# Kernel optimization log

Hardware: AMD Instinct MI355X
Metric: run time of the kernel (lower is better)

The kernel has to match this reference:

```python
import jax, jax.numpy as jnp
import numpy as np

N_HEADS = 16
D_MODEL = 1024
TOTAL = 8192
N_SEQ = 8
SEQ_LEN = TOTAL // N_SEQ


def setup_inputs() -> dict:
    key = jax.random.key(0)
    ks = jax.random.split(key, 12)
    f = jnp.float32
    d = D_MODEL
    inp = {
        "query": jax.random.normal(ks[0], (TOTAL, d), f),
        "key": jax.random.normal(ks[1], (TOTAL, d), f),
        "value": jax.random.normal(ks[2], (TOTAL, d), f),
        "seq_lengths_q": jnp.full((N_SEQ,), SEQ_LEN, jnp.int64 if jax.config.jax_enable_x64 else jnp.int32),
        "seq_lengths_kv": jnp.full((N_SEQ,), SEQ_LEN, jnp.int64 if jax.config.jax_enable_x64 else jnp.int32),
        "Wq": jax.random.normal(ks[3], (d, d), f) * 0.02,
        "bq": jnp.zeros((d,), f),
        "Wk": jax.random.normal(ks[4], (d, d), f) * 0.02,
        "bk": jnp.zeros((d,), f),
        "Wv": jax.random.normal(ks[5], (d, d), f) * 0.02,
        "bv": jnp.zeros((d,), f),
        "Wo": jax.random.normal(ks[6], (d, d), f) * 0.02,
        "bo": jnpp if False else jnp.zeros((d,), f),
    }
    return inp


def reference(query, key, value, seq_lengths_q, seq_lengths_kv, Wq, bq, Wk, bk, Wv, bv, Wo, bo):
    Tq, d = query.shape
    Tkv = key.shape[0]
    H = N_HEADS
    Dh = d // H
    B = seq_lengths_q.shape[0]
    Lq = Tq // B  # equal-length packed sequences
    Lkv = Tkv // B
    scale = 1.0 / jnp.sqrt(jnp.asarray(Dh, query.dtype))

    # torch Linear: x @ W.T + b
    Q = (query @ Wq.T + bq).reshape(H, Tq, Dh)   # NOTE: raw view, no transpose
    K = (key @ Wk.T + bk).reshape(H, Tkv, Dh)    # (replicates original's view semantics)
    V = (value @ Wv.T + bv).reshape(H, Tkv, Dh)

    # Block-diagonal mask over equal-length sequences == per-block attention.
    Qb = Q.reshape(H, B, Lq, Dh)
    Kb = K.reshape(H, B, Lkv, Dh)
    Vb = V.reshape(H, B, Lkv, Dh)

    scores = jnp.einsum("hbqd,hbkd->hbqk", Qb, Kb) * scale  # [H,B,Lq,Lkv]
    probs = jax.nn.softmax(scores, axis=-1)
    attn = jnp.einsum("hbqk,hbkd->hbqd", probs, Vb)          # [H,B,Lq,Dh]

    attn = attn.reshape(H, Tq, Dh).reshape(Tq, d)  # matches .view(total_q, d_model)
    out = attn @ Wo.T + bo
    return out
```

## Files before the change

kernel.cpp:

```cpp
#include <hip/hip_runtime.h>
#include <hip/hip_bf16.h>

#define TOTAL   8192
#define DMODEL  1024
#define NHEADS  16
#define NSEQ    8
#define DH      64

typedef float  f32x4 __attribute__((ext_vector_type(4)));
typedef short  s16x8 __attribute__((ext_vector_type(8)));
typedef unsigned short u16;
typedef u16    u16x8 __attribute__((ext_vector_type(8)));
typedef unsigned u32x2 __attribute__((ext_vector_type(2)));

__device__ __forceinline__ u16 f2bf_rne(float x) {
  union { float f; unsigned u; } v; v.f = x;
  unsigned r = v.u + 0x7FFFu + ((v.u >> 16) & 1u);
  return (u16)(r >> 16);
}

__device__ __forceinline__ void async_cp16(const u16* g, u16* l) {
  __builtin_amdgcn_global_load_lds(
      (const __attribute__((address_space(1))) unsigned int*)g,
      (__attribute__((address_space(3))) unsigned int*)l, 16, 0, 0);
}

__device__ __forceinline__ void cvt8_one(const float* __restrict__ src,
                                         u16* __restrict__ dst, long i) {
  float4 a = *reinterpret_cast<const float4*>(src + i);
  float4 b = *reinterpret_cast<const float4*>(src + i + 4);
  u16x8 o;
  o[0] = f2bf_rne(a.x); o[1] = f2bf_rne(a.y); o[2] = f2bf_rne(a.z); o[3] = f2bf_rne(a.w);
  o[4] = f2bf_rne(b.x); o[5] = f2bf_rne(b.y); o[6] = f2bf_rne(b.z); o[7] = f2bf_rne(b.w);
  *reinterpret_cast<u16x8*>(dst + i) = o;
}

__global__ __launch_bounds__(256) void cvt8(const float* __restrict__ src,
                                            u16* __restrict__ dst) {
  cvt8_one(src, dst, ((long)blockIdx.x * 256 + threadIdx.x) * 8);
}

__global__ __launch_bounds__(256) void cvt8_w4(const float* __restrict__ w0,
                                               const float* __restrict__ w1,
                                               const float* __restrict__ w2,
                                               const float* __restrict__ w3,
                                               u16* __restrict__ dst) {
  const float* srcs[4] = {w0, w1, w2, w3};
  cvt8_one(srcs[blockIdx.y], dst + (long)blockIdx.y * (DMODEL * (long)DMODEL),
           ((long)blockIdx.x * 256 + threadIdx.x) * 8);
}

__global__ __launch_bounds__(256) void cvt8_x3(const float* __restrict__ x0,
                                               const float* __restrict__ x1,
                                               const float* __restrict__ x2,
                                               u16* __restrict__ dst) {
  const float* srcs[3] = {x0, x1, x2};
  cvt8_one(srcs[blockIdx.y], dst + (long)blockIdx.y * (TOTAL * (long)DMODEL),
           ((long)blockIdx.x * 256 + threadIdx.x) * 8);
}

template<bool OUT_BF16>
__device__ __forceinline__ void gemm256_core(const u16* __restrict__ A,
                                             const u16* __restrict__ B,
                                             const float* __restrict__ bias,
                                             void* __restrict__ Cp,
                                             long bm0, long bn0, u16* lds) {
  const int tid  = threadIdx.x;
  const int lane = tid & 63;
  const int wv   = tid >> 6;
  const int quad = lane >> 4;
  const int m16  = lane & 15;
  const int wm   = (wv >> 1) * 64;
  const int wn   = (wv & 1) * 64;

  const int l8   = lane >> 3;
  const int slot = (lane & 7) ^ l8;
  const long g_lane = (long)l8 * DMODEL + slot * 8;
  const u16* Ap = A + (bm0 + wv * 32) * (long)DMODEL + g_lane;
  const u16* Bp = B + (bn0 + wv * 16) * (long)DMODEL + g_lane;
  u16* ldsA = lds + wv * (4 * 512);
  u16* ldsB = lds + 16384 + wv * (2 * 512);

  const int swz0 = ((quad * 16)      ^ ((m16 & 7) << 4)) >> 1;
  const int swz1 = ((64 + quad * 16) ^ ((m16 & 7) << 4)) >> 1;
  const int aro = (wm + m16) * 64;
  const int bro = 16384 + (wn + m16) * 64;

  f32x4 acc[4][4] = {};

#define STAGE_A(buf, kt) do {                                       \
    _Pragma("unroll")                                               \
    for (int al = 0; al < 4; al++)                                  \
      async_cp16(Ap + (long)(kt) * 64 + al * (8 * DMODEL),          \
                 ldsA + (buf) * 24576 + al * 512);                  \
  } while (0)
#define STAGE_B(buf, kt) do {                                       \
    _Pragma("unroll")                                               \
    for (int bl = 0; bl < 2; bl++)                                  \
      async_cp16(Bp + (long)(kt) * 64 + bl * (8 * DMODEL),          \
                 ldsB + (buf) * 24576 + bl * 512);                  \
  } while (0)

  STAGE_A(0, 0); STAGE_B(0, 0);
  STAGE_A(1, 1); STAGE_B(1, 1);

  #pragma unroll
  for (int t = 0; t < 16; t++) {
    const int cur = t % 3;
    const int stg = (t + 2) % 3;
    if (t < 15) asm volatile("s_waitcnt vmcnt(6)" ::: "memory");
    else        asm volatile("s_waitcnt vmcnt(0)" ::: "memory");
    __builtin_amdgcn_s_barrier();
    asm volatile("" ::: "memory");

    const u16* lb = lds + cur * 24576;

    if (t < 14) STAGE_A(stg, t + 2);
    s16x8 bf[4][2], af[2][2];
    #pragma unroll
    for (int n = 0; n < 4; n++) {
      bf[n][0] = *(const s16x8*)&lb[bro + n * 1024 + swz0];
      bf[n][1] = *(const s16x8*)&lb[bro + n * 1024 + swz1];
    }
    #pragma unroll
    for (int i = 0; i < 2; i++) {
      af[i][0] = *(const s16x8*)&lb[aro + i * 1024 + swz0];
      af[i][1] = *(const s16x8*)&lb[aro + i * 1024 + swz1];
    }
    asm volatile("s_waitcnt lgkmcnt(0)" ::: "memory");
    __builtin_amdgcn_sched_barrier(0);
    __builtin_amdgcn_s_setprio(1);
    #pragma unroll
    for (int i = 0; i < 2; i++)
      #pragma unroll
      for (int n = 0; n < 4; n++) {
        acc[i][n] = __builtin_amdgcn_mfma_f32_16x16x32_bf16(af[i][0], bf[n][0], acc[i][n], 0, 0, 0);
        acc[i][n] = __builtin_amdgcn_mfma_f32_16x16x32_bf16(af[i][1], bf[n][1], acc[i][n], 0, 0, 0);
      }
    __builtin_amdgcn_s_setprio(0);
    __builtin_amdgcn_s_barrier();

    if (t < 14) STAGE_B(stg, t + 2);
    s16x8 ag[2][2];
    #pragma unroll
    for (int i = 0; i < 2; i++) {
      ag[i][0] = *(const s16x8*)&lb[aro + (i + 2) * 1024 + swz0];
      ag[i][1] = *(const s16x8*)&lb[aro + (i + 2) * 1024 + swz1];
    }
    asm volatile("s_waitcnt lgkmcnt(0)" ::: "memory");
    __builtin_amdgcn_sched_barrier(0);
    __builtin_amdgcn_s_setprio(1);
    #pragma unroll
    for (int i = 0; i < 2; i++)
      #pragma unroll
      for (int n = 0; n < 4; n++) {
        acc[i + 2][n] = __builtin_amdgcn_mfma_f32_16x16x32_bf16(ag[i][0], bf[n][0], acc[i + 2][n], 0, 0, 0);
        acc[i + 2][n] = __builtin_amdgcn_mfma_f32_16x16x32_bf16(ag[i][1], bf[n][1], acc[i + 2][n], 0, 0, 0);
      }
    __builtin_amdgcn_s_setprio(0);
  }
#undef STAGE_A
#undef STAGE_B

  #pragma unroll
  for (int n = 0; n < 4; n++) {
    const long col = bn0 + wn + n * 16 + m16;
    const float bj = bias[col];
    #pragma unroll
    for (int i = 0; i < 4; i++) {
      const long row0 = bm0 + wm + i * 16 + quad * 4;
      #pragma unroll
      for (int r = 0; r < 4; r++) {
        float v = acc[i][n][r] + bj;
        if constexpr (OUT_BF16)
          ((u16*)Cp)[(row0 + r) * DMODEL + col] = f2bf_rne(v);
        else
          ((float*)Cp)[(row0 + r) * DMODEL + col] = v;
      }
    }
  }
}

__device__ __forceinline__ void decode_wg(int x, long& bm0, long& bn0) {
  const int wg = (x & 7) * 32 + (x >> 3);
  bm0 = (long)(wg >> 3) * 256;
  bn0 = (long)(wg & 7) * 128;
}

template<bool OUT_BF16>
__global__ __launch_bounds__(512, 2) void gemm256_nt(const u16* __restrict__ A,
                                                     const u16* __restrict__ B,
                                                     const float* __restrict__ bias,
                                                     void* __restrict__ Cp) {
  __shared__ __align__(1024) u16 lds[3 * 24576];
  long bm0, bn0;
  decode_wg(blockIdx.x, bm0, bn0);
  gemm256_core<OUT_BF16>(A, B, bias, Cp, bm0, bn0, lds);
}

__global__ __launch_bounds__(512, 2) void gemm256_qkv(const u16* __restrict__ X3,
                                                      const u16* __restrict__ W3,
                                                      const float* __restrict__ bq,
                                                      const float* __restrict__ bk,
                                                      const float* __restrict__ bv,
                                                      u16* __restrict__ QKV) {
  __shared__ __align__(1024) u16 lds[3 * 24576];
  const int z = blockIdx.y;
  const float* bias = (z == 0) ? bq : (z == 1) ? bk : bv;
  long bm0, bn0;
  decode_wg(blockIdx.x, bm0, bn0);
  gemm256_core<true>(X3 + (long)z * (TOTAL * (long)DMODEL),
                     W3 + (long)z * (DMODEL * (long)DMODEL),
                     bias,
                     QKV + (long)z * (TOTAL * (long)DMODEL),
                     bm0, bn0, lds);
}

__global__ __launch_bounds__(256) void transpose_v(const u16* __restrict__ Vbf,
                                                   u16* __restrict__ Vt) {
  constexpr int TP = 72;
  __shared__ u16 tile[64 * TP];
  const int tid = threadIdx.x;
  const long base = (long)blockIdx.y * 65536;
  const int kt = blockIdx.x;
  {
    int k = tid >> 2, dh0 = (tid & 3) * 16;
    const u16* g = Vbf + base + (long)(kt * 64 + k) * 64 + dh0;
    u16x8 a = ((const u16x8*)g)[0];
    u16x8 b = ((const u16x8*)g)[1];
    #pragma unroll
    for (int i = 0; i < 8; i++) tile[(dh0 + i) * TP + k] = a[i];
    #pragma unroll
    for (int i = 0; i < 8; i++) tile[(dh0 + 8 + i) * TP + k] = b[i];
  }
  __syncthreads();
  {
    int dh = tid >> 2, k0 = (tid & 3) * 16;
    u16x8 a = *(const u16x8*)&tile[dh * TP + k0];
    u16x8 b = *(const u16x8*)&tile[dh * TP + k0 + 8];
    u16* g = Vt + base + (long)dh * 1024 + kt * 64 + k0;
    ((u16x8*)g)[0] = a;
    ((u16x8*)g)[1] = b;
  }
}

__global__ __launch_bounds__(256) void attn_kernel(const u16* __restrict__ Qbf,
                                                   const u16* __restrict__ Kbf,
                                                   const u16* __restrict__ Vt,
                                                   u16* __restrict__ Obf) {
  constexpr int KP = 72;
  __shared__ u16 Ks[64 * KP];
  __shared__ u16 Vs[64 * KP];
  __shared__ u16 Es[4 * 32 * KP];
  const int tid  = threadIdx.x;
  const int lane = tid & 63;
  const int wv   = tid >> 6;
  const int quad = lane >> 4;
  const int m16  = lane & 15;
  const int qt   = blockIdx.y;
  const long base = (long)blockIdx.x * 65536;

  const int qrow0 = qt * 128 + wv * 32;
  s16x8 aq[2][2];
  #pragma unroll
  for (int g = 0; g < 2; g++)
    #pragma unroll
    for (int s = 0; s < 2; s++)
      aq[g][s] = *(const s16x8*)(Qbf + base + (long)(qrow0 + g * 16 + m16) * 64 + s * 32 + quad * 8);

  f32x4 acc_o[2][4] = {};
  f32x4 acc_d[2] = {};

  union { u16x8 u; s16x8 s; } onesu;
  u16 ov = (m16 == 0) ? (u16)0x3F80 : (u16)0;
  #pragma unroll
  for (int i = 0; i < 8; i++) onesu.u[i] = ov;
  const s16x8 bones = onesu.s;

  const float SC = 0.125f * 1.44269504088896340736f;
  const int sr = tid >> 2;
  const int sk = (tid & 3) * 16;

  const u16* gK = Kbf + base + (long)sr * 64 + sk;
  const u16* gV = Vt  + base + (long)sr * 1024 + sk;
  u16x8 kra = ((const u16x8*)gK)[0], krb = ((const u16x8*)gK)[1];
  u16x8 vra = ((const u16x8*)gV)[0], vrb = ((const u16x8*)gV)[1];

  for (int nt = 0; nt < 16; nt++) {
    *(u16x8*)&Ks[sr * KP + sk]     = kra;
    *(u16x8*)&Ks[sr * KP + sk + 8] = krb;
    *(u16x8*)&Vs[sr * KP + sk]     = vra;
    *(u16x8*)&Vs[sr * KP + sk + 8] = vrb;
    __syncthreads();
    if (nt < 15) {
      const u16* nK = gK + (nt + 1) * 4096;
      const u16* nV = gV + (nt + 1) * 64;
      kra = ((const u16x8*)nK)[0]; krb = ((const u16x8*)nK)[1];
      vra = ((const u16x8*)nV)[0]; vrb = ((const u16x8*)nV)[1];
    }

    #pragma unroll
    for (int mt = 0; mt < 4; mt++) {
      const int krow = (mt * 16 + m16) * KP;
      s16x8 kf0 = *(const s16x8*)&Ks[krow + quad * 8];
      s16x8 kf1 = *(const s16x8*)&Ks[krow + 32 + quad * 8];
      #pragma unroll
      for (int g = 0; g < 2; g++) {
        f32x4 s = {0.f, 0.f, 0.f, 0.f};
        s = __builtin_amdgcn_mfma_f32_16x16x32_bf16(kf0, aq[g][0], s, 0, 0, 0);
        s = __builtin_amdgcn_mfma_f32_16x16x32_bf16(kf1, aq[g][1], s, 0, 0, 0);
        float e0 = __builtin_amdgcn_exp2f(s[0] * SC);
        float e1 = __builtin_amdgcn_exp2f(s[1] * SC);
        float e2 = __builtin_amdgcn_exp2f(s[2] * SC);
        float e3 = __builtin_amdgcn_exp2f(s[3] * SC);
        unsigned p0 = (unsigned)f2bf_rne(e0) | ((unsigned)f2bf_rne(e1) << 16);
        unsigned p1 = (unsigned)f2bf_rne(e2) | ((unsigned)f2bf_rne(e3) << 16);
        u32x2 w; w.x = p0; w.y = p1;
        *(u32x2*)&Es[(wv * 32 + g * 16 + m16) * KP + mt * 16 + quad * 4] = w;
      }
    }
    asm volatile("s_waitcnt lgkmcnt(0)" ::: "memory");
    __builtin_amdgcn_sched_barrier(0);

    s16x8 ae[2][2];
    #pragma unroll
    for (int g = 0; g < 2; g++) {
      ae[g][0] = *(const s16x8*)&Es[(wv * 32 + g * 16 + m16) * KP + quad * 8];
      ae[g][1] = *(const s16x8*)&Es[(wv * 32 + g * 16 + m16) * KP + 32 + quad * 8];
    }
    __builtin_amdgcn_s_setprio(1);
    #pragma unroll
    for (int n = 0; n < 4; n++) {
      s16x8 bv0 = *(const s16x8*)&Vs[(n * 16 + m16) * KP + quad * 8];
      s16x8 bv1 = *(const s16x8*)&Vs[(n * 16 + m16) * KP + 32 + quad * 8];
      #pragma unroll
      for (int g = 0; g < 2; g++) {
        acc_o[g][n] = __builtin_amdgcn_mfma_f32_16x16x32_bf16(ae[g][0], bv0, acc_o[g][n], 0, 0, 0);
        acc_o[g][n] = __builtin_amdgcn_mfma_f32_16x16x32_bf16(ae[g][1], bv1, acc_o[g][n], 0, 0, 0);
      }
    }
    #pragma unroll
    for (int g = 0; g < 2; g++) {
      acc_d[g] = __builtin_amdgcn_mfma_f32_16x16x32_bf16(ae[g][0], bones, acc_d[g], 0, 0, 0);
      acc_d[g] = __builtin_amdgcn_mfma_f32_16x16x32_bf16(ae[g][1], bones, acc_d[g], 0, 0, 0);
    }
    __builtin_amdgcn_s_setprio(0);
    __syncthreads();
  }

  #pragma unroll
  for (int g = 0; g < 2; g++)
    #pragma unroll
    for (int r = 0; r < 4; r++) {
      float d = __shfl(acc_d[g][r], lane & 48);
      float rinv = 1.0f / d;
      const long orow = base + (long)(qrow0 + g * 16 + quad * 4 + r) * 64;
      #pragma unroll
      for (int n = 0; n < 4; n++)
        Obf[orow + n * 16 + m16] = f2bf_rne(acc_o[g][n][r] * rinv);
    }
}

extern "C" void kernel_launch(void* const* d_in, const int* in_sizes, int n_in,
                              void* d_out, int out_size, void* d_ws, size_t ws_size,
                              hipStream_t stream) {
  const float* query = (const float*)d_in[0];
  const float* key_  = (const float*)d_in[1];
  const float* value = (const float*)d_in[2];
  const float* Wq = (const float*)d_in[5];
  const float* bq = (const float*)d_in[6];
  const float* Wk = (const float*)d_in[7];
  const float* bk = (const float*)d_in[8];
  const float* Wv = (const float*)d_in[9];
  const float* bv = (const float*)d_in[10];
  const float* Wo = (const float*)d_in[11];
  const float* bo = (const float*)d_in[12];

  char* ws = (char*)d_ws;
  const size_t FUSED_NEED = 104ull << 20;

  if (ws_size >= FUSED_NEED) {
    u16* Wbf = (u16*)(ws);
    u16* QKV = (u16*)(ws + (8l << 20));
    u16* Qbf = QKV;
    u16* Kbf = QKV + 1 * (TOTAL * (long)DMODEL);
    u16* Vbf = QKV + 2 * (TOTAL * (long)DMODEL);
    u16* X3  = (u16*)(ws + (56l << 20));
    u16* Vt  = X3;
    u16* Obf = Vbf;

    cvt8_w4<<<dim3(512, 4), 256, 0, stream>>>(Wq, Wk, Wv, Wo, Wbf);
    cvt8_x3<<<dim3(4096, 3), 256, 0, stream>>>(query, key_, value, X3);
    gemm256_qkv<<<dim3(256, 3), 512, 0, stream>>>(X3, Wbf, bq, bk, bv, QKV);
    transpose_v<<<dim3(16, 128), 256, 0, stream>>>(Vbf, Vt);
    attn_kernel<<<dim3(128, 8), 256, 0, stream>>>(Qbf, Kbf, Vt, Obf);
    gemm256_nt<false><<<dim3(256), 512, 0, stream>>>(Obf, Wbf + 3 * 1048576, bo, (float*)d_out);
  } else {
    u16* Wbf = (u16*)(ws);
    u16* Xbf = (u16*)(ws + (8l << 20));
    u16* Qbf = (u16*)(ws + (24l << 20));
    u16* Kbf = (u16*)(ws + (40l << 20));
    u16* Vbf = (u16*)(ws + (56l << 20));
    u16* Vt  = Xbf;
    u16* Obf = Vbf;

    cvt8_w4<<<dim3(512, 4), 256, 0, stream>>>(Wq, Wk, Wv, Wo, Wbf);
    cvt8<<<4096, 256, 0, stream>>>(query, Xbf);
    gemm256_nt<true><<<dim3(256), 512, 0, stream>>>(Xbf, Wbf + 0 * 1048576, bq, Qbf);
    cvt8<<<4096, 256, 0, stream>>>(key_, Xbf);
    gemm256_nt<true><<<dim3(256), 512, 0, stream>>>(Xbf, Wbf + 1 * 1048576, bk, Kbf);
    cvt8<<<4096, 256, 0, stream>>>(value, Xbf);
    gemm256_nt<true><<<dim3(256), 512, 0, stream>>>(Xbf, Wbf + 2 * 1048576, bv, Vbf);
    transpose_v<<<dim3(16, 128), 256, 0, stream>>>(Vbf, Vt);
    attn_kernel<<<dim3(128, 8), 256, 0, stream>>>(Qbf, Kbf, Vt, Obf);
    gemm256_nt<false><<<dim3(256), 512, 0, stream>>>(Obf, Wbf + 3 * 1048576, bo, (float*)d_out);
  }
}
```

Measured before the change: 318.6 us.

## Keep softmax probabilities in registers and feed PV MFMA directly

The exponentiated score fragments are now packed into registers and used directly as the A operand of 16x16x16 bf16 MFMAs against V. This removes the LDS round trip through the Es scratch buffer, its waitcnt and sched barrier, and the extra LDS footprint. In exchange it uses the smaller K=16 MFMA shape, doubling the PV instruction count, and it issues more narrow V fragment reads from LDS.

```diff
diff --git a/kernel.cpp b/kernel.cpp
--- a/kernel.cpp
+++ b/kernel.cpp
@@ -9,9 +9,9 @@
 
 typedef float  f32x4 __attribute__((ext_vector_type(4)));
 typedef short  s16x8 __attribute__((ext_vector_type(8)));
+typedef short  s16x4 __attribute__((ext_vector_type(4)));
 typedef unsigned short u16;
 typedef u16    u16x8 __attribute__((ext_vector_type(8)));
-typedef unsigned u32x2 __attribute__((ext_vector_type(2)));
 
 __device__ __forceinline__ u16 f2bf_rne(float x) {
   union { float f; unsigned u; } v; v.f = x;
@@ -23,6 +23,19 @@
   __builtin_amdgcn_global_load_lds(
       (const __attribute__((address_space(1))) unsigned int*)g,
       (__attribute__((address_space(3))) unsigned int*)l, 16, 0, 0);
+}
+
+__device__ __forceinline__ f32x4 mfma16_bf16(s16x4 a, s16x4 b, f32x4 c) {
+#if __has_builtin(__builtin_amdgcn_mfma_f32_16x16x16bf16_1k)
+  return __builtin_amdgcn_mfma_f32_16x16x16bf16_1k(a, b, c, 0, 0, 0);
+#elif __has_builtin(__builtin_amdgcn_mfma_f32_16x16x16_bf16)
+  return __builtin_amdgcn_mfma_f32_16x16x16_bf16(a, b, c, 0, 0, 0);
+#else
+  f32x4 d;
+  asm("v_mfma_f32_16x16x16_bf16 %0, %1, %2, %3"
+      : "=v"(d) : "v"(a), "v"(b), "v"(c));
+  return d;
+#endif
 }
 
 __device__ __forceinline__ void cvt8_one(const float* __restrict__ src,
@@ -251,7 +264,6 @@
   constexpr int KP = 72;
   __shared__ u16 Ks[64 * KP];
   __shared__ u16 Vs[64 * KP];
-  __shared__ u16 Es[4 * 32 * KP];
   const int tid  = threadIdx.x;
   const int lane = tid & 63;
   const int wv   = tid >> 6;
@@ -271,11 +283,11 @@
   f32x4 acc_o[2][4] = {};
   f32x4 acc_d[2] = {};
 
-  union { u16x8 u; s16x8 s; } onesu;
+  union { u16 u[4]; s16x4 s; } onesu;
   u16 ov = (m16 == 0) ? (u16)0x3F80 : (u16)0;
   #pragma unroll
-  for (int i = 0; i < 8; i++) onesu.u[i] = ov;
-  const s16x8 bones = onesu.s;
+  for (int i = 0; i < 4; i++) onesu.u[i] = ov;
+  const s16x4 bones4 = onesu.s;
 
   const float SC = 0.125f * 1.44269504088896340736f;
   const int sr = tid >> 2;
@@ -299,11 +311,16 @@
       vra = ((const u16x8*)nV)[0]; vrb = ((const u16x8*)nV)[1];
     }
 
+    __builtin_amdgcn_s_setprio(1);
     #pragma unroll
     for (int mt = 0; mt < 4; mt++) {
       const int krow = (mt * 16 + m16) * KP;
       s16x8 kf0 = *(const s16x8*)&Ks[krow + quad * 8];
       s16x8 kf1 = *(const s16x8*)&Ks[krow + 32 + quad * 8];
+      s16x4 bv4[4];
+      #pragma unroll
+      for (int n = 0; n < 4; n++)
+        bv4[n] = *(const s16x4*)&Vs[(n * 16 + m16) * KP + mt * 16 + quad * 4];
       #pragma unroll
       for (int g = 0; g < 2; g++) {
         f32x4 s = {0.f, 0.f, 0.f, 0.f};
@@ -313,36 +330,14 @@
         float e1 = __builtin_amdgcn_exp2f(s[1] * SC);
         float e2 = __builtin_amdgcn_exp2f(s[2] * SC);
         float e3 = __builtin_amdgcn_exp2f(s[3] * SC);
-        unsigned p0 = (unsigned)f2bf_rne(e0) | ((unsigned)f2bf_rne(e1) << 16);
-        unsigned p1 = (unsigned)f2bf_rne(e2) | ((unsigned)f2bf_rne(e3) << 16);
-        u32x2 w; w.x = p0; w.y = p1;
-        *(u32x2*)&Es[(wv * 32 + g * 16 + m16) * KP + mt * 16 + quad * 4] = w;
+        union { unsigned u[2]; s16x4 s; } ea;
+        ea.u[0] = (unsigned)f2bf_rne(e0) | ((unsigned)f2bf_rne(e1) << 16);
+        ea.u[1] = (unsigned)f2bf_rne(e2) | ((unsigned)f2bf_rne(e3) << 16);
+        #pragma unroll
+        for (int n = 0; n < 4; n++)
+          acc_o[g][n] = mfma16_bf16(ea.s, bv4[n], acc_o[g][n]);
+        acc_d[g] = mfma16_bf16(ea.s, bones4, acc_d[g]);
       }
-    }
-    asm volatile("s_waitcnt lgkmcnt(0)" ::: "memory");
-    __builtin_amdgcn_sched_barrier(0);
-
-    s16x8 ae[2][2];
-    #pragma unroll
-    for (int g = 0; g < 2; g++) {
-      ae[g][0] = *(const s16x8*)&Es[(wv * 32 + g * 16 + m16) * KP + quad * 8];
-      ae[g][1] = *(const s16x8*)&Es[(wv * 32 + g * 16 + m16) * KP + 32 + quad * 8];
-    }
-    __builtin_amdgcn_s_setprio(1);
-    #pragma unroll
-    for (int n = 0; n < 4; n++) {
-      s16x8 bv0 = *(const s16x8*)&Vs[(n * 16 + m16) * KP + quad * 8];
-      s16x8 bv1 = *(const s16x8*)&Vs[(n * 16 + m16) * KP + 32 + quad * 8];
-      #pragma unroll
-      for (int g = 0; g < 2; g++) {
-        acc_o[g][n] = __builtin_amdgcn_mfma_f32_16x16x32_bf16(ae[g][0], bv0, acc_o[g][n], 0, 0, 0);
-        acc_o[g][n] = __builtin_amdgcn_mfma_f32_16x16x32_bf16(ae[g][1], bv1, acc_o[g][n], 0, 0, 0);
-      }
-    }
-    #pragma unroll
-    for (int g = 0; g < 2; g++) {
-      acc_d[g] = __builtin_amdgcn_mfma_f32_16x16x32_bf16(ae[g][0], bones, acc_d[g], 0, 0, 0);
-      acc_d[g] = __builtin_amdgcn_mfma_f32_16x16x32_bf16(ae[g][1], bones, acc_d[g], 0, 0, 0);
     }
     __builtin_amdgcn_s_setprio(0);
     __syncthreads();
```

Result: no change. 319.9 us (+0.4%).
